# Optimization experiments

Hardware: AMD Instinct MI355X
Metric: run time of the kernel (lower is better)

Reference implementation:

```python
import jax, jax.numpy as jnp
import numpy as np

NUM_EXPERTS = 8
HIDDEN = 1024
INTERMEDIATE = 2816
TOTAL_TOKENS = 4096  # 512 tokens per expert


def setup_inputs() -> dict:
    key = jax.random.key(0)
    k_x, k1, k2, k3 = jax.random.split(key, 4)
    hiddens = jax.random.normal(k_x, (TOTAL_TOKENS, HIDDEN), dtype=jnp.float32)
    # tokens assumed pre-sorted by expert; equal-sized groups here
    batch_sizes = jnp.full((NUM_EXPERTS,), TOTAL_TOKENS // NUM_EXPERTS, dtype=jnp.int64)
    w1_weight = jax.random.normal(k1, (NUM_EXPERTS, HIDDEN, INTERMEDIATE), dtype=jnp.float32)
    w2_weight = jax.random.normal(k2, (NUM_EXPERTS, INTERMEDIATE, HIDDEN), dtype=jnp.float32)
    w3_weight = jax.random.normal(k3, (NUM_EXPERTS, HIDDEN, INTERMEDIATE), dtype=jnp.float32)
    return {
        "hiddens": hiddens,
        "w1_weight": w1_weight,
        "w2_weight": w2_weight,
        "w3_weight": w3_weight,
        "batch_sizes": batch_sizes,
    }


def _grouped_moe(hiddens, w1, w2, w3, batch_sizes):
    """Grouped SwiGLU FFN: tokens are contiguous per expert (sizes = batch_sizes).

    Jit-safe formulation: map each token to its expert id, then run one masked
    dense GEMM trio per expert (small fixed expert count). Zero rows contribute
    exactly zero (silu(0)*0 == 0), so no final masking of the output is needed.
    """
    num_experts = w1.shape[0]
    total_tokens = hiddens.shape[0]
    bounds = jnp.cumsum(batch_sizes)  # [E] exclusive-right boundaries
    expert_ids = jnp.searchsorted(bounds, jnp.arange(total_tokens), side="right")  # [T]
    out = jnp.zeros((total_tokens, w2.shape[-1]), dtype=hiddens.dtype)
    for e in range(num_experts):
        mask = (expert_ids == e)[:, None]  # [T, 1]
        xe = jnp.where(mask, hiddens, 0)   # zero out other experts' tokens
        up = jax.nn.silu(xe @ w1[e]) * (xe @ w3[e])  # [T, F] SwiGLU
        out = out + up @ w2[e]             # [T, H]
    return out


def reference(hiddens, w1_weight, w2_weight, w3_weight, batch_sizes):
    return _grouped_moe(hiddens, w1_weight, w2_weight, w3_weight, batch_sizes)
```

## Files before the change

kernel.cpp:

```cpp
#include <hip/hip_runtime.h>
#include <hip/hip_bf16.h>

#define NE 8
#define HD 1024
#define ID 2816
#define TT 4096
#define BM 128
#define BK 32
#define BN1 64
#define BN2 64
#define NTH 256
#define MAXMT (TT / BM + NE)

typedef __attribute__((ext_vector_type(4))) float f32x4;
typedef __attribute__((ext_vector_type(8))) short s16x8;
typedef __attribute__((ext_vector_type(4))) short s16x4;

__device__ __forceinline__ unsigned int f2bfpk(float lo, float hi) {
  float2 t; t.x = lo; t.y = hi;
  union { __hip_bfloat162 h2; unsigned int u; } cv;
  cv.h2 = __float22bfloat162_rn(t);
  return cv.u;
}

__device__ __forceinline__ bool map_tile(const void* bsp, int mt, int& e,
                                         int& mstart, int& rowend) {
  const int* w = (const int*)bsp;
  bool is64 = (w[1] == 0) && (w[3] == 0) && (w[5] == 0) && (w[7] == 0) &&
              ((w[0] | w[2] | w[4] | w[6]) != 0);
  long long start = 0;
  int rem = mt;
  for (int i = 0; i < NE; ++i) {
    long long b = is64 ? ((const long long*)bsp)[i] : (long long)w[i];
    if (b < 0) b = 0;
    int tiles = (int)((b + BM - 1) / BM);
    if (rem < tiles) {
      long long m0 = start + (long long)rem * BM;
      long long me = start + b;
      if (m0 >= TT) return false;
      if (me > TT) me = TT;
      e = i; mstart = (int)m0; rowend = (int)me;
      return true;
    }
    rem -= tiles;
    start += b;
  }
  return false;
}

__global__ __launch_bounds__(NTH, 2) void moe_gemm1(
    const float* __restrict__ x, const float* __restrict__ w1,
    const float* __restrict__ w3, const void* __restrict__ bsp,
    __hip_bfloat16* __restrict__ up) {
  __shared__ __align__(16) char As[2][BM * 80];
  __shared__ __align__(16) char B1s[2][BN1 * 72];
  __shared__ __align__(16) char B3s[2][BN1 * 72];

  const int NWG = (ID / BN1) * MAXMT;
  int bid = blockIdx.x;
  int logical = (bid & 7) * (NWG >> 3) + (bid >> 3);
  int mt = logical % MAXMT;
  int nt = logical / MAXMT;
  int e, mstart, rowend;
  if (!map_tile(bsp, mt, e, mstart, rowend)) return;
  const int n0 = nt * BN1;
  const int tid = threadIdx.x;

  const int lane = tid & 63;
  const int wv = tid >> 6;
  const int wr = wv >> 1, wc = wv & 1;
  const int q = lane >> 4, r16 = lane & 15;

  const int a_k4 = (tid & 7) * 4;
  const int a_r0 = tid >> 3;
  const int b_n = tid & 63;
  const int b_kp0 = tid >> 6;

  const float* w1p = w1 + (size_t)e * HD * ID + n0 + b_n;
  const float* w3p = w3 + (size_t)e * HD * ID + n0 + b_n;

  f32x4 acc1[4][2], acc3[4][2];
#pragma unroll
  for (int i = 0; i < 4; ++i)
#pragma unroll
    for (int j = 0; j < 2; ++j) { acc1[i][j] = (f32x4)0.f; acc3[i][j] = (f32x4)0.f; }

  f32x4 xa[4];
  float wa1[4][2], wa3[4][2];

  auto load_tile = [&](int kb) {
#pragma unroll
    for (int it = 0; it < 4; ++it) {
      int gm = mstart + a_r0 + it * 32;
      f32x4 v = (f32x4)0.f;
      if (gm < rowend) v = *(const f32x4*)(x + (size_t)gm * HD + kb + a_k4);
      xa[it] = v;
    }
#pragma unroll
    for (int i = 0; i < 4; ++i) {
      int k = kb + 2 * (b_kp0 + i * 4);
      const float* p1 = w1p + (size_t)k * ID;
      wa1[i][0] = p1[0]; wa1[i][1] = p1[ID];
      const float* p3 = w3p + (size_t)k * ID;
      wa3[i][0] = p3[0]; wa3[i][1] = p3[ID];
    }
  };
  auto store_tile = [&](int buf) {
#pragma unroll
    for (int it = 0; it < 4; ++it) {
      int r = a_r0 + it * 32;
      unsigned long long p =
          (unsigned long long)f2bfpk(xa[it][0], xa[it][1]) |
          ((unsigned long long)f2bfpk(xa[it][2], xa[it][3]) << 32);
      *(unsigned long long*)(As[buf] + r * 80 + a_k4 * 2) = p;
    }
#pragma unroll
    for (int i = 0; i < 4; ++i) {
      int kp = b_kp0 + i * 4;
      *(unsigned int*)(B1s[buf] + b_n * 72 + kp * 4) = f2bfpk(wa1[i][0], wa1[i][1]);
      *(unsigned int*)(B3s[buf] + b_n * 72 + kp * 4) = f2bfpk(wa3[i][0], wa3[i][1]);
    }
  };
  auto compute = [&](int buf) {
    s16x8 a[4], b1[2], b3[2];
#pragma unroll
    for (int i = 0; i < 4; ++i)
      a[i] = *(const s16x8*)(As[buf] + (wr * 64 + i * 16 + r16) * 80 + q * 16);
#pragma unroll
    for (int j = 0; j < 2; ++j) {
      const char* p1 = B1s[buf] + (wc * 32 + j * 16 + r16) * 72 + q * 16;
      s16x4 l1 = *(const s16x4*)p1, h1 = *(const s16x4*)(p1 + 8);
      b1[j] = __builtin_shufflevector(l1, h1, 0, 1, 2, 3, 4, 5, 6, 7);
      const char* p3 = B3s[buf] + (wc * 32 + j * 16 + r16) * 72 + q * 16;
      s16x4 l3 = *(const s16x4*)p3, h3 = *(const s16x4*)(p3 + 8);
      b3[j] = __builtin_shufflevector(l3, h3, 0, 1, 2, 3, 4, 5, 6, 7);
    }
#pragma unroll
    for (int i = 0; i < 4; ++i)
#pragma unroll
      for (int j = 0; j < 2; ++j) {
        acc1[i][j] = __builtin_amdgcn_mfma_f32_16x16x32_bf16(a[i], b1[j], acc1[i][j], 0, 0, 0);
        acc3[i][j] = __builtin_amdgcn_mfma_f32_16x16x32_bf16(a[i], b3[j], acc3[i][j], 0, 0, 0);
      }
  };

  const int NK = HD / BK;
  load_tile(0);
  store_tile(0);
  for (int kt = 0; kt < NK; ++kt) {
    __syncthreads();
    if (kt + 1 < NK) load_tile((kt + 1) * BK);
    compute(kt & 1);
    if (kt + 1 < NK) store_tile((kt + 1) & 1);
  }

#pragma unroll
  for (int i = 0; i < 4; ++i)
#pragma unroll
    for (int r = 0; r < 4; ++r) {
      int gm = mstart + wr * 64 + i * 16 + q * 4 + r;
      if (gm < rowend) {
#pragma unroll
        for (int j = 0; j < 2; ++j) {
          float v1 = acc1[i][j][r], v3 = acc3[i][j][r];
          float s = v1 / (1.f + __expf(-v1));
          up[(size_t)gm * ID + n0 + wc * 32 + j * 16 + r16] = __float2bfloat16(s * v3);
        }
      }
    }
}

__global__ __launch_bounds__(NTH, 2) void moe_gemm2(
    const __hip_bfloat16* __restrict__ up, const float* __restrict__ w2,
    const void* __restrict__ bsp, float* __restrict__ out) {
  __shared__ __align__(16) char As[2][BM * 80];
  __shared__ __align__(16) char Bs[2][BN2 * 72];

  const int NWG = (HD / BN2) * MAXMT;
  int bid = blockIdx.x;
  int logical = (bid & 7) * (NWG >> 3) + (bid >> 3);
  int mt = logical % MAXMT;
  int nt = logical / MAXMT;
  int e, mstart, rowend;
  if (!map_tile(bsp, mt, e, mstart, rowend)) return;
  const int n0 = nt * BN2;
  const int tid = threadIdx.x;

  const int lane = tid & 63;
  const int wv = tid >> 6;
  const int wr = wv >> 1, wc = wv & 1;
  const int q = lane >> 4, r16 = lane & 15;

  const int a_k8 = (tid & 3) * 8;
  const int a_r0 = tid >> 2;
  const int b_n = tid & 63;
  const int b_kp0 = tid >> 6;

  const float* w2p = w2 + (size_t)e * ID * HD + n0 + b_n;

  f32x4 acc[4][2];
#pragma unroll
  for (int i = 0; i < 4; ++i)
#pragma unroll
    for (int j = 0; j < 2; ++j) acc[i][j] = (f32x4)0.f;

  s16x8 ua[2];
  float wa[4][2];

  auto load_tile = [&](int kb) {
#pragma unroll
    for (int it = 0; it < 2; ++it) {
      int gm = mstart + a_r0 + it * 64;
      s16x8 v = (s16x8)0;
      if (gm < rowend) v = *(const s16x8*)(up + (size_t)gm * ID + kb + a_k8);
      ua[it] = v;
    }
#pragma unroll
    for (int i = 0; i < 4; ++i) {
      int k = kb + 2 * (b_kp0 + i * 4);
      const float* p = w2p + (size_t)k * HD;
      wa[i][0] = p[0]; wa[i][1] = p[HD];
    }
  };
  auto store_tile = [&](int buf) {
#pragma unroll
    for (int it = 0; it < 2; ++it) {
      int r = a_r0 + it * 64;
      *(s16x8*)(As[buf] + r * 80 + a_k8 * 2) = ua[it];
    }
#pragma unroll
    for (int i = 0; i < 4; ++i) {
      int kp = b_kp0 + i * 4;
      *(unsigned int*)(Bs[buf] + b_n * 72 + kp * 4) = f2bfpk(wa[i][0], wa[i][1]);
    }
  };
  auto compute = [&](int buf) {
    s16x8 a[4], b[2];
#pragma unroll
    for (int i = 0; i < 4; ++i)
      a[i] = *(const s16x8*)(As[buf] + (wr * 64 + i * 16 + r16) * 80 + q * 16);
#pragma unroll
    for (int j = 0; j < 2; ++j) {
      const char* p = Bs[buf] + (wc * 32 + j * 16 + r16) * 72 + q * 16;
      s16x4 lo = *(const s16x4*)p, hi = *(const s16x4*)(p + 8);
      b[j] = __builtin_shufflevector(lo, hi, 0, 1, 2, 3, 4, 5, 6, 7);
    }
#pragma unroll
    for (int i = 0; i < 4; ++i)
#pragma unroll
      for (int j = 0; j < 2; ++j)
        acc[i][j] = __builtin_amdgcn_mfma_f32_16x16x32_bf16(a[i], b[j], acc[i][j], 0, 0, 0);
  };

  const int NK = ID / BK;
  load_tile(0);
  store_tile(0);
  for (int kt = 0; kt < NK; ++kt) {
    __syncthreads();
    if (kt + 1 < NK) load_tile((kt + 1) * BK);
    compute(kt & 1);
    if (kt + 1 < NK) store_tile((kt + 1) & 1);
  }

#pragma unroll
  for (int i = 0; i < 4; ++i)
#pragma unroll
    for (int r = 0; r < 4; ++r) {
      int gm = mstart + wr * 64 + i * 16 + q * 4 + r;
      if (gm < rowend) {
#pragma unroll
        for (int j = 0; j < 2; ++j)
          out[(size_t)gm * HD + n0 + wc * 32 + j * 16 + r16] = acc[i][j][r];
      }
    }
}

extern "C" void kernel_launch(void* const* d_in, const int* in_sizes, int n_in,
                              void* d_out, int out_size, void* d_ws, size_t ws_size,
                              hipStream_t stream) {
  const float* x = (const float*)d_in[0];
  const float* w1 = (const float*)d_in[1];
  const float* w2 = (const float*)d_in[2];
  const float* w3 = (const float*)d_in[3];
  const void* bs = d_in[4];
  float* out = (float*)d_out;
  __hip_bfloat16* up = (__hip_bfloat16*)d_ws;

  hipMemsetAsync(d_out, 0, (size_t)out_size * sizeof(float), stream);

  dim3 blk(NTH);
  moe_gemm1<<<dim3((ID / BN1) * MAXMT), blk, 0, stream>>>(x, w1, w3, bs, up);
  moe_gemm2<<<dim3((HD / BN2) * MAXMT), blk, 0, stream>>>(up, w2, bs, out);
}
```

Baseline: 215.6 us.

## Pre-convert activations to bf16 and deepen register prefetch with two-stage pipeline

Adds a separate kernel that converts the fp32 input activations to bf16 once, so the first GEMM loads bf16 A tiles instead of converting fp32 per tile in every workgroup. Both GEMMs now prefetch two K-tiles ahead into alternating register sets, use incrementing pointers instead of recomputed indices, and replace __syncthreads with a lgkmcnt wait plus s_barrier. This is meant to hide global load latency and cut redundant conversion and address math, at the cost of more registers, an extra launch and extra workspace traffic.

Measured after the change: 195.3 us. -9.4%, faster.

```diff
diff --git a/kernel.cpp b/kernel.cpp
--- a/kernel.cpp
+++ b/kernel.cpp
@@ -21,6 +21,11 @@
   union { __hip_bfloat162 h2; unsigned int u; } cv;
   cv.h2 = __float22bfloat162_rn(t);
   return cv.u;
+}
+
+__device__ __forceinline__ void lds_barrier() {
+  asm volatile("s_waitcnt lgkmcnt(0)" ::: "memory");
+  __builtin_amdgcn_s_barrier();
 }
 
 __device__ __forceinline__ bool map_tile(const void* bsp, int mt, int& e,
@@ -48,8 +53,23 @@
   return false;
 }
 
+__global__ __launch_bounds__(NTH) void cvt_x(const float* __restrict__ x,
+                                             __hip_bfloat16* __restrict__ xb) {
+  size_t i = ((size_t)blockIdx.x * NTH + threadIdx.x) * 8;
+  f32x4 v0 = *(const f32x4*)(x + i);
+  f32x4 v1 = *(const f32x4*)(x + i + 4);
+  s16x8 o;
+  unsigned int p0 = f2bfpk(v0[0], v0[1]), p1 = f2bfpk(v0[2], v0[3]);
+  unsigned int p2 = f2bfpk(v1[0], v1[1]), p3 = f2bfpk(v1[2], v1[3]);
+  o[0] = (short)(p0 & 0xffff); o[1] = (short)(p0 >> 16);
+  o[2] = (short)(p1 & 0xffff); o[3] = (short)(p1 >> 16);
+  o[4] = (short)(p2 & 0xffff); o[5] = (short)(p2 >> 16);
+  o[6] = (short)(p3 & 0xffff); o[7] = (short)(p3 >> 16);
+  *(s16x8*)((unsigned short*)xb + i) = o;
+}
+
 __global__ __launch_bounds__(NTH, 2) void moe_gemm1(
-    const float* __restrict__ x, const float* __restrict__ w1,
+    const __hip_bfloat16* __restrict__ xbf, const float* __restrict__ w1,
     const float* __restrict__ w3, const void* __restrict__ bsp,
     __hip_bfloat16* __restrict__ up) {
   __shared__ __align__(16) char As[2][BM * 80];
@@ -71,13 +91,17 @@
   const int wr = wv >> 1, wc = wv & 1;
   const int q = lane >> 4, r16 = lane & 15;
 
-  const int a_k4 = (tid & 7) * 4;
-  const int a_r0 = tid >> 3;
+  const int a_k8 = (tid & 3) * 8;
+  const int a_r0 = tid >> 2;
   const int b_n = tid & 63;
   const int b_kp0 = tid >> 6;
 
-  const float* w1p = w1 + (size_t)e * HD * ID + n0 + b_n;
-  const float* w3p = w3 + (size_t)e * HD * ID + n0 + b_n;
+  const bool ok0 = (mstart + a_r0) < rowend;
+  const bool ok1 = (mstart + a_r0 + 64) < rowend;
+
+  const __hip_bfloat16* xc = xbf + (size_t)(mstart + a_r0) * HD + a_k8;
+  const float* w1c = w1 + (size_t)e * HD * ID + n0 + b_n + (size_t)(2 * b_kp0) * ID;
+  const float* w3c = w3 + (size_t)e * HD * ID + n0 + b_n + (size_t)(2 * b_kp0) * ID;
 
   f32x4 acc1[4][2], acc3[4][2];
 #pragma unroll
@@ -85,53 +109,44 @@
 #pragma unroll
     for (int j = 0; j < 2; ++j) { acc1[i][j] = (f32x4)0.f; acc3[i][j] = (f32x4)0.f; }
 
-  f32x4 xa[4];
-  float wa1[4][2], wa3[4][2];
-
-  auto load_tile = [&](int kb) {
-#pragma unroll
-    for (int it = 0; it < 4; ++it) {
-      int gm = mstart + a_r0 + it * 32;
-      f32x4 v = (f32x4)0.f;
-      if (gm < rowend) v = *(const f32x4*)(x + (size_t)gm * HD + kb + a_k4);
-      xa[it] = v;
-    }
+  s16x8 A0[2], A1[2];
+  float W1a[4][2], W3a[4][2], W1b[4][2], W3b[4][2];
+
+  auto load_t = [&](s16x8* A, float (*W1_)[2], float (*W3_)[2]) {
+    A[0] = ok0 ? *(const s16x8*)xc : (s16x8)0;
+    A[1] = ok1 ? *(const s16x8*)(xc + (size_t)64 * HD) : (s16x8)0;
+    xc += BK;
 #pragma unroll
     for (int i = 0; i < 4; ++i) {
-      int k = kb + 2 * (b_kp0 + i * 4);
-      const float* p1 = w1p + (size_t)k * ID;
-      wa1[i][0] = p1[0]; wa1[i][1] = p1[ID];
-      const float* p3 = w3p + (size_t)k * ID;
-      wa3[i][0] = p3[0]; wa3[i][1] = p3[ID];
-    }
-  };
-  auto store_tile = [&](int buf) {
-#pragma unroll
-    for (int it = 0; it < 4; ++it) {
-      int r = a_r0 + it * 32;
-      unsigned long long p =
-          (unsigned long long)f2bfpk(xa[it][0], xa[it][1]) |
-          ((unsigned long long)f2bfpk(xa[it][2], xa[it][3]) << 32);
-      *(unsigned long long*)(As[buf] + r * 80 + a_k4 * 2) = p;
-    }
+      const float* p1 = w1c + (size_t)(8 * i) * ID;
+      W1_[i][0] = p1[0]; W1_[i][1] = p1[ID];
+      const float* p3 = w3c + (size_t)(8 * i) * ID;
+      W3_[i][0] = p3[0]; W3_[i][1] = p3[ID];
+    }
+    w1c += (size_t)BK * ID; w3c += (size_t)BK * ID;
+  };
+  auto store_t = [&](char* As_, char* B1_, char* B3_, const s16x8* A,
+                     const float (*W1_)[2], const float (*W3_)[2]) {
+    *(s16x8*)(As_ + a_r0 * 80 + a_k8 * 2) = A[0];
+    *(s16x8*)(As_ + (a_r0 + 64) * 80 + a_k8 * 2) = A[1];
 #pragma unroll
     for (int i = 0; i < 4; ++i) {
       int kp = b_kp0 + i * 4;
-      *(unsigned int*)(B1s[buf] + b_n * 72 + kp * 4) = f2bfpk(wa1[i][0], wa1[i][1]);
-      *(unsigned int*)(B3s[buf] + b_n * 72 + kp * 4) = f2bfpk(wa3[i][0], wa3[i][1]);
-    }
-  };
-  auto compute = [&](int buf) {
+      *(unsigned int*)(B1_ + b_n * 72 + kp * 4) = f2bfpk(W1_[i][0], W1_[i][1]);
+      *(unsigned int*)(B3_ + b_n * 72 + kp * 4) = f2bfpk(W3_[i][0], W3_[i][1]);
+    }
+  };
+  auto compute_t = [&](const char* As_, const char* B1_, const char* B3_) {
     s16x8 a[4], b1[2], b3[2];
 #pragma unroll
     for (int i = 0; i < 4; ++i)
-      a[i] = *(const s16x8*)(As[buf] + (wr * 64 + i * 16 + r16) * 80 + q * 16);
+      a[i] = *(const s16x8*)(As_ + (wr * 64 + i * 16 + r16) * 80 + q * 16);
 #pragma unroll
     for (int j = 0; j < 2; ++j) {
-      const char* p1 = B1s[buf] + (wc * 32 + j * 16 + r16) * 72 + q * 16;
+      const char* p1 = B1_ + (wc * 32 + j * 16 + r16) * 72 + q * 16;
       s16x4 l1 = *(const s16x4*)p1, h1 = *(const s16x4*)(p1 + 8);
       b1[j] = __builtin_shufflevector(l1, h1, 0, 1, 2, 3, 4, 5, 6, 7);
-      const char* p3 = B3s[buf] + (wc * 32 + j * 16 + r16) * 72 + q * 16;
+      const char* p3 = B3_ + (wc * 32 + j * 16 + r16) * 72 + q * 16;
       s16x4 l3 = *(const s16x4*)p3, h3 = *(const s16x4*)(p3 + 8);
       b3[j] = __builtin_shufflevector(l3, h3, 0, 1, 2, 3, 4, 5, 6, 7);
     }
@@ -145,13 +160,21 @@
   };
 
   const int NK = HD / BK;
-  load_tile(0);
-  store_tile(0);
-  for (int kt = 0; kt < NK; ++kt) {
-    __syncthreads();
-    if (kt + 1 < NK) load_tile((kt + 1) * BK);
-    compute(kt & 1);
-    if (kt + 1 < NK) store_tile((kt + 1) & 1);
+  load_t(A0, W1a, W3a);
+  load_t(A1, W1b, W3b);
+  store_t(As[0], B1s[0], B3s[0], A0, W1a, W3a);
+  lds_barrier();
+  for (int kt = 0; kt < NK; kt += 2) {
+    if (kt + 2 < NK) load_t(A0, W1a, W3a);
+    compute_t(As[0], B1s[0], B3s[0]);
+    store_t(As[1], B1s[1], B3s[1], A1, W1b, W3b);
+    lds_barrier();
+    if (kt + 3 < NK) load_t(A1, W1b, W3b);
+    compute_t(As[1], B1s[1], B3s[1]);
+    if (kt + 2 < NK) {
+      store_t(As[0], B1s[0], B3s[0], A0, W1a, W3a);
+      lds_barrier();
+    }
   }
 
 #pragma unroll
@@ -196,7 +219,11 @@
   const int b_n = tid & 63;
   const int b_kp0 = tid >> 6;
 
-  const float* w2p = w2 + (size_t)e * ID * HD + n0 + b_n;
+  const bool ok0 = (mstart + a_r0) < rowend;
+  const bool ok1 = (mstart + a_r0 + 64) < rowend;
+
+  const __hip_bfloat16* uc = up + (size_t)(mstart + a_r0) * ID + a_k8;
+  const float* w2c = w2 + (size_t)e * ID * HD + n0 + b_n + (size_t)(2 * b_kp0) * HD;
 
   f32x4 acc[4][2];
 #pragma unroll
@@ -204,44 +231,37 @@
 #pragma unroll
     for (int j = 0; j < 2; ++j) acc[i][j] = (f32x4)0.f;
 
-  s16x8 ua[2];
-  float wa[4][2];
-
-  auto load_tile = [&](int kb) {
-#pragma unroll
-    for (int it = 0; it < 2; ++it) {
-      int gm = mstart + a_r0 + it * 64;
-      s16x8 v = (s16x8)0;
-      if (gm < rowend) v = *(const s16x8*)(up + (size_t)gm * ID + kb + a_k8);
-      ua[it] = v;
-    }
+  s16x8 A0[2], A1[2];
+  float Wa[4][2], Wb[4][2];
+
+  auto load_t = [&](s16x8* A, float (*W_)[2]) {
+    A[0] = ok0 ? *(const s16x8*)uc : (s16x8)0;
+    A[1] = ok1 ? *(const s16x8*)(uc + (size_t)64 * ID) : (s16x8)0;
+    uc += BK;
 #pragma unroll
     for (int i = 0; i < 4; ++i) {
-      int k = kb + 2 * (b_kp0 + i * 4);
-      const float* p = w2p + (size_t)k * HD;
-      wa[i][0] = p[0]; wa[i][1] = p[HD];
-    }
-  };
-  auto store_tile = [&](int buf) {
-#pragma unroll
-    for (int it = 0; it < 2; ++it) {
-      int r = a_r0 + it * 64;
-      *(s16x8*)(As[buf] + r * 80 + a_k8 * 2) = ua[it];
-    }
+      const float* p = w2c + (size_t)(8 * i) * HD;
+      W_[i][0] = p[0]; W_[i][1] = p[HD];
+    }
+    w2c += (size_t)BK * HD;
+  };
+  auto store_t = [&](char* As_, char* B_, const s16x8* A, const float (*W_)[2]) {
+    *(s16x8*)(As_ + a_r0 * 80 + a_k8 * 2) = A[0];
+    *(s16x8*)(As_ + (a_r0 + 64) * 80 + a_k8 * 2) = A[1];
 #pragma unroll
     for (int i = 0; i < 4; ++i) {
       int kp = b_kp0 + i * 4;
-      *(unsigned int*)(Bs[buf] + b_n * 72 + kp * 4) = f2bfpk(wa[i][0], wa[i][1]);
-    }
-  };
-  auto compute = [&](int buf) {
+      *(unsigned int*)(B_ + b_n * 72 + kp * 4) = f2bfpk(W_[i][0], W_[i][1]);
+    }
+  };
+  auto compute_t = [&](const char* As_, const char* B_) {
     s16x8 a[4], b[2];
 #pragma unroll
     for (int i = 0; i < 4; ++i)
-      a[i] = *(const s16x8*)(As[buf] + (wr * 64 + i * 16 + r16) * 80 + q * 16);
+      a[i] = *(const s16x8*)(As_ + (wr * 64 + i * 16 + r16) * 80 + q * 16);
 #pragma unroll
     for (int j = 0; j < 2; ++j) {
-      const char* p = Bs[buf] + (wc * 32 + j * 16 + r16) * 72 + q * 16;
+      const char* p = B_ + (wc * 32 + j * 16 + r16) * 72 + q * 16;
       s16x4 lo = *(const s16x4*)p, hi = *(const s16x4*)(p + 8);
       b[j] = __builtin_shufflevector(lo, hi, 0, 1, 2, 3, 4, 5, 6, 7);
     }
@@ -253,13 +273,21 @@
   };
 
   const int NK = ID / BK;
-  load_tile(0);
-  store_tile(0);
-  for (int kt = 0; kt < NK; ++kt) {
-    __syncthreads();
-    if (kt + 1 < NK) load_tile((kt + 1) * BK);
-    compute(kt & 1);
-    if (kt + 1 < NK) store_tile((kt + 1) & 1);
+  load_t(A0, Wa);
+  load_t(A1, Wb);
+  store_t(As[0], Bs[0], A0, Wa);
+  lds_barrier();
+  for (int kt = 0; kt < NK; kt += 2) {
+    if (kt + 2 < NK) load_t(A0, Wa);
+    compute_t(As[0], Bs[0]);
+    store_t(As[1], Bs[1], A1, Wb);
+    lds_barrier();
+    if (kt + 3 < NK) load_t(A1, Wb);
+    compute_t(As[1], Bs[1]);
+    if (kt + 2 < NK) {
+      store_t(As[0], Bs[0], A0, Wa);
+      lds_barrier();
+    }
   }
 
 #pragma unroll
@@ -284,11 +312,13 @@
   const float* w3 = (const float*)d_in[3];
   const void* bs = d_in[4];
   float* out = (float*)d_out;
-  __hip_bfloat16* up = (__hip_bfloat16*)d_ws;
+  __hip_bfloat16* xbf = (__hip_bfloat16*)d_ws;
+  __hip_bfloat16* up = (__hip_bfloat16*)((char*)d_ws + (size_t)TT * HD * 2);
 
   hipMemsetAsync(d_out, 0, (size_t)out_size * sizeof(float), stream);
 
   dim3 blk(NTH);
-  moe_gemm1<<<dim3((ID / BN1) * MAXMT), blk, 0, stream>>>(x, w1, w3, bs, up);
+  cvt_x<<<dim3(TT * HD / (8 * NTH)), blk, 0, stream>>>(x, xbf);
+  moe_gemm1<<<dim3((ID / BN1) * MAXMT), blk, 0, stream>>>(xbf, w1, w3, bs, up);
   moe_gemm2<<<dim3((HD / BN2) * MAXMT), blk, 0, stream>>>(up, w2, bs, out);
 }
```
